# Kernel tuning notes

Measured on AMD Instinct MI355X. Metric: run time of the kernel, lower is better.

## Reference

```python
import jax, jax.numpy as jnp
import numpy as np

B, T, D = 128, 2048, 256


def setup_inputs() -> dict:
    key = jax.random.key(0)
    ks = jax.random.split(key, 6)
    s = 1.0 / np.sqrt(D)  # kaiming-uniform-ish scale for bias-free Linear
    return {
        "x": jax.random.normal(ks[0], (B, T, D), jnp.float32),
        "W_in": jax.random.normal(ks[1], (D, D), jnp.float32) * s,
        "W_select": jax.random.normal(ks[2], (D, D), jnp.float32) * s,
        "W_gate": jax.random.normal(ks[3], (D, D), jnp.float32) * s,
        "W_out": jax.random.normal(ks[4], (D, D), jnp.float32) * s,
        "W_delta": jax.random.normal(ks[5], (D, D), jnp.float32) * s,
        "log_a": jnp.zeros((D,), jnp.float32),  # module inits log_a = zeros
    }


def _diag_recurrence(decay, update):
    # state_t = decay_t * state_{t-1} + update_t, state_{-1} = 0 (zero-init fast path)
    # First-order linear recurrence as an associative scan:
    # (a1,b1) o (a2,b2) = (a1*a2, a2*b1 + b2)
    def combine(c1, c2):
        a1, b1 = c1
        a2, b2 = c2
        return a1 * a2, a2 * b1 + b2

    _, states = jax.lax.associative_scan(combine, (decay, update), axis=1)
    return states  # (B, T, D)


def reference(x, W_in, W_select, W_gate, W_out, W_delta, log_a):
    # selective diag-SSM (a_mode='diag'):
    #   delta  = softplus(delta_proj(x))                  timestep / selectivity
    #   decay  = exp(-delta * exp(log_a))                 in (0, 1]
    #   update = delta * sigmoid(select_proj(x)) * in_proj(x)
    #   states = scan(state = decay*state + update)
    #   y      = states * silu(gate_proj(x)); out = out_proj(y)
    delta = jax.nn.softplus(jnp.einsum("btd,ed->bte", x, W_delta))
    decay = jnp.exp(-delta * jnp.exp(log_a))
    u = jnp.einsum("btd,ed->bte", x, W_in)
    sel = jax.nn.sigmoid(jnp.einsum("btd,ed->bte", x, W_select))
    update = delta * sel * u
    states = _diag_recurrence(decay, update)
    gate = jax.nn.silu(jnp.einsum("btd,ed->bte", x, W_gate))
    return jnp.einsum("btd,ed->bte", states * gate, W_out)
```

## Files before the change

kernel.cpp:

```cpp
#include <hip/hip_runtime.h>
#include <hip/hip_bf16.h>
#include <hip/hip_fp16.h>
#include <math.h>


typedef __attribute__((ext_vector_type(8))) short s16x8;
typedef __attribute__((ext_vector_type(4))) float f32x4;

#define D_DIM 256
#define T_DIM 2048
#define B_DIM 128
#define NCHUNK2 32
#define CLEN 128

__device__ __forceinline__ unsigned short f2bf(float f) {
    union { float f; unsigned int u; } v; v.f = f;
    unsigned int r = v.u + 0x7fffu + ((v.u >> 16) & 1u);
    return (unsigned short)(r >> 16);
}
__device__ __forceinline__ float bf2f(unsigned short s) {
    union { unsigned int u; float f; } v; v.u = ((unsigned int)s) << 16;
    return v.f;
}
__device__ __forceinline__ void gload_lds16(const void* g, void* l) {
    __builtin_amdgcn_global_load_lds(
        (const __attribute__((address_space(1))) unsigned int*)g,
        (__attribute__((address_space(3))) unsigned int*)l, 16, 0, 0);
}

__global__ __launch_bounds__(256) void prep_kernel(
    const float* __restrict__ W_in, const float* __restrict__ W_select,
    const float* __restrict__ W_gate, const float* __restrict__ W_out,
    const float* __restrict__ W_delta, const float* __restrict__ log_a,
    unsigned short* __restrict__ Wb, float* __restrict__ ea)
{
    int i = blockIdx.x * 256 + threadIdx.x;
    if (i < 4 * 65536) {
        int row = i >> 8, k = i & 255;
        int n = row >> 2, w = row & 3;
        const float* src = (w == 0) ? W_delta : (w == 1) ? W_select
                         : (w == 2) ? W_in    : W_gate;
        Wb[i] = f2bf(src[n * 256 + k]);
    } else if (i < 5 * 65536) {
        Wb[i] = f2bf(W_out[i - 4 * 65536]);
    } else if (i < 5 * 65536 + 256) {
        int j = i - 5 * 65536;
        ea[j] = expf(log_a[j]);
    }
}

__global__ __launch_bounds__(256) void xcast_kernel(
    const float* __restrict__ x, unsigned short* __restrict__ xb)
{
    size_t i = ((size_t)blockIdx.x * 256 + threadIdx.x) * 8;
    float4 p0 = *(const float4*)(x + i);
    float4 p1 = *(const float4*)(x + i + 4);
    s16x8 a;
    a[0] = (short)f2bf(p0.x); a[1] = (short)f2bf(p0.y);
    a[2] = (short)f2bf(p0.z); a[3] = (short)f2bf(p0.w);
    a[4] = (short)f2bf(p1.x); a[5] = (short)f2bf(p1.y);
    a[6] = (short)f2bf(p1.z); a[7] = (short)f2bf(p1.w);
    *(s16x8*)(xb + i) = a;
}

__global__ __launch_bounds__(256, 3) void gemm_fused_kernel(
    const unsigned short* __restrict__ xb, const unsigned short* __restrict__ Wcat,
    const float* __restrict__ ea,
    __half2* __restrict__ du, unsigned short* __restrict__ gate,
    float* __restrict__ cA, float* __restrict__ cS)
{
    __shared__ char lds[32768];
    int bid = blockIdx.x;
    int wg  = (bid & 7) * 2048 + (bid >> 3);
    int mt  = wg >> 3;
    int nt  = wg & 7;
    int mbase = mt * 128;
    int nb = nt * 128;
    int tid = threadIdx.x, lane = tid & 63, wid = tid >> 6;
    int l16 = lane & 15, lk = lane >> 4;
    int wr = wid >> 1, wc = wid & 1;

    const unsigned short* xg  = xb   + (size_t)mbase * D_DIM;
    const unsigned short* wgp = Wcat + (size_t)nb * D_DIM;

    int se0 = tid, se1 = 256 + tid;
    int sr0 = se0 >> 2, sg0 = (se0 & 3) ^ ((sr0 >> 1) & 3);
    int sr1 = se1 >> 2, sg1 = (se1 & 3) ^ ((sr1 >> 1) & 3);

    float eav[4];
#pragma unroll
    for (int nf = 0; nf < 4; ++nf)
        eav[nf] = ea[nt * 32 + wc * 16 + nf * 4 + lk];
    asm volatile("s_waitcnt vmcnt(0)" ::: "memory");
    __builtin_amdgcn_sched_barrier(0);

#define STAGE(BUFB, KB)                                                     \
    {                                                                        \
        gload_lds16(xg  + (size_t)sr0 * D_DIM + (KB) + sg0 * 8,              \
                    lds + (BUFB) + se0 * 16);                                \
        gload_lds16(xg  + (size_t)sr1 * D_DIM + (KB) + sg1 * 8,              \
                    lds + (BUFB) + se1 * 16);                                \
        gload_lds16(wgp + (size_t)sr0 * D_DIM + (KB) + sg0 * 8,              \
                    lds + (BUFB) + 8192 + se0 * 16);                         \
        gload_lds16(wgp + (size_t)sr1 * D_DIM + (KB) + sg1 * 8,              \
                    lds + (BUFB) + 8192 + se1 * 16);                         \
    }

    f32x4 acc[4][4] = {};

#define COMPUTE(BUFB)                                                        \
    {                                                                        \
        s16x8 xf[4], wf[4];                                                  \
        _Pragma("unroll")                                                    \
        for (int mf = 0; mf < 4; ++mf) {                                     \
            int row = wr * 64 + mf * 16 + l16;                               \
            int g = lk ^ ((row >> 1) & 3);                                   \
            xf[mf] = *(const s16x8*)(lds + (BUFB) + row * 64 + g * 16);      \
        }                                                                    \
        _Pragma("unroll")                                                    \
        for (int nf = 0; nf < 4; ++nf) {                                     \
            int row = wc * 64 + nf * 16 + l16;                               \
            int g = lk ^ ((row >> 1) & 3);                                   \
            wf[nf] = *(const s16x8*)(lds + (BUFB) + 8192 + row * 64 + g * 16);\
        }                                                                    \
        _Pragma("unroll")                                                    \
        for (int nf = 0; nf < 4; ++nf)                                       \
            _Pragma("unroll")                                                \
            for (int mf = 0; mf < 4; ++mf)                                   \
                acc[mf][nf] = __builtin_amdgcn_mfma_f32_16x16x32_bf16(       \
                    wf[nf], xf[mf], acc[mf][nf], 0, 0, 0);                   \
    }

    STAGE(0, 0);
#pragma unroll 1
    for (int p = 0; p < 4; ++p) {
        STAGE(16384, (2 * p + 1) * 32);
        __builtin_amdgcn_sched_barrier(0);
        asm volatile("s_waitcnt vmcnt(4)" ::: "memory");
        __builtin_amdgcn_s_barrier();
        __builtin_amdgcn_sched_barrier(0);
        COMPUTE(0);
        __builtin_amdgcn_sched_barrier(0);
        asm volatile("s_waitcnt lgkmcnt(0)" ::: "memory");
        __builtin_amdgcn_s_barrier();
        __builtin_amdgcn_sched_barrier(0);
        if (p < 3) {
            STAGE(0, (2 * p + 2) * 32);
            __builtin_amdgcn_sched_barrier(0);
            asm volatile("s_waitcnt vmcnt(4)" ::: "memory");
        } else {
            __builtin_amdgcn_sched_barrier(0);
            asm volatile("s_waitcnt vmcnt(0)" ::: "memory");
        }
        __builtin_amdgcn_s_barrier();
        __builtin_amdgcn_sched_barrier(0);
        COMPUTE(16384);
        __builtin_amdgcn_sched_barrier(0);
        asm volatile("s_waitcnt lgkmcnt(0)" ::: "memory");
        __builtin_amdgcn_s_barrier();
        __builtin_amdgcn_sched_barrier(0);
    }
#undef STAGE
#undef COMPUTE

#pragma unroll
    for (int nf = 0; nf < 4; ++nf) {
        int n = nt * 32 + wc * 16 + nf * 4 + lk;
        float ean = eav[nf];
        float A[4], S[4];
#pragma unroll
        for (int mf = 0; mf < 4; ++mf) {
            int m = mbase + wr * 64 + mf * 16 + l16;
            float zd = acc[mf][nf][0];
            float zs = acc[mf][nf][1];
            float zi = acc[mf][nf][2];
            float zg = acc[mf][nf][3];
            float e = __expf(zd);
            float delta = (zd > 15.f) ? zd : __logf(1.f + e);
            float dec = __expf(-delta * ean);
            float sel = 1.f / (1.f + __expf(-zs));
            float upd = delta * sel * zi;
            float g   = zg / (1.f + __expf(-zg));
            du[(size_t)m * D_DIM + n] = __floats2half2_rn(dec, upd);
            gate[(size_t)m * D_DIM + n] = f2bf(g);
            A[mf] = dec;
            S[mf] = upd;
        }
#pragma unroll
        for (int d = 1; d < 16; d <<= 1) {
            bool upper = (l16 & d);
#pragma unroll
            for (int mf = 0; mf < 4; ++mf) {
                float Ap = __shfl_xor(A[mf], d, 64);
                float Sp = __shfl_xor(S[mf], d, 64);
                float Se = upper ? Sp : S[mf];
                float Al = upper ? A[mf] : Ap;
                float Sl = upper ? S[mf] : Sp;
                S[mf] = fmaf(Al, Se, Sl);
                A[mf] = A[mf] * Ap;
            }
        }
        float cAe = A[0], cSe = S[0];
#pragma unroll
        for (int mf = 1; mf < 4; ++mf) {
            cSe = fmaf(A[mf], cSe, S[mf]);
            cAe *= A[mf];
        }
        if (l16 == 0) {
            int hc = mt * 2 + wr;
            cA[hc * D_DIM + n] = cAe;
            cS[hc * D_DIM + n] = cSe;
        }
    }
}

__global__ __launch_bounds__(256) void scan2_kernel(
    const float* __restrict__ cA, const float* __restrict__ cS,
    float* __restrict__ carry)
{
    int b = blockIdx.x;
    int d = threadIdx.x;
    float s = 0.f;
    for (int c = 0; c < NCHUNK2; ++c) {
        int idx = (b * NCHUNK2 + c) * D_DIM + d;
        carry[idx] = s;
        s = fmaf(cA[idx], s, cS[idx]);
    }
}

__global__ __launch_bounds__(256) void scan_out_kernel(
    const __half2* __restrict__ du, const unsigned short* __restrict__ gate,
    const float* __restrict__ carry, const unsigned short* __restrict__ Wo,
    float* __restrict__ out)
{
    __shared__ unsigned short yls[128 * 256];
    int b = blockIdx.x >> 4;
    int c = blockIdx.x & 15;
    int tid = threadIdx.x;

    {
        int d = tid;
        size_t base = ((size_t)b * T_DIM + (size_t)c * CLEN) * D_DIM + d;
        float s = carry[(b * NCHUNK2 + c * 2) * D_DIM + d];
        int dlo = d & 7, dch = d >> 3;
#pragma unroll 4
        for (int t = 0; t < CLEN; ++t) {
            __half2 v = du[base + (size_t)t * D_DIM];
            float dc = __low2float(v);
            float up = __high2float(v);
            s = fmaf(dc, s, up);
            float g = bf2f(gate[base + (size_t)t * D_DIM]);
            int off = t * 256 + ((dch ^ (t & 7)) << 3) + dlo;
            yls[off] = f2bf(s * g);
        }
    }
    __syncthreads();

    int lane = tid & 63, wid = tid >> 6;
    int l16 = lane & 15;
    int lkc = lane >> 4;
    int m0 = (wid >> 1) * 64;
    size_t rbase = (size_t)b * T_DIM + (size_t)c * CLEN;
    int r0 = lkc * 4;

    for (int nblk = 0; nblk < 2; ++nblk) {
        int n0 = (wid & 1) * 64 + nblk * 128;
        f32x4 acc[4][4] = {};
        for (int ks = 0; ks < 8; ++ks) {
            int kb = ks * 32 + lkc * 8;
            s16x8 yf[4];
#pragma unroll
            for (int mf = 0; mf < 4; ++mf) {
                int row = m0 + mf * 16 + l16;
                int chunk = (ks * 4 + lkc) ^ (row & 7);
                yf[mf] = *(const s16x8*)&yls[row * 256 + chunk * 8];
            }
#pragma unroll
            for (int nf = 0; nf < 4; ++nf) {
                s16x8 wfr = *(const s16x8*)(Wo + (size_t)(n0 + nf * 16 + l16) * D_DIM + kb);
#pragma unroll
                for (int mf = 0; mf < 4; ++mf)
                    acc[mf][nf] = __builtin_amdgcn_mfma_f32_16x16x32_bf16(
                        wfr, yf[mf], acc[mf][nf], 0, 0, 0);
            }
        }
#pragma unroll
        for (int mf = 0; mf < 4; ++mf) {
            size_t rowg = rbase + m0 + mf * 16 + l16;
#pragma unroll
            for (int nf = 0; nf < 4; ++nf) {
                int n = n0 + nf * 16 + r0;
                *(f32x4*)(out + rowg * D_DIM + n) = acc[mf][nf];
            }
        }
    }
}

extern "C" void kernel_launch(void* const* d_in, const int* in_sizes, int n_in,
                              void* d_out, int out_size, void* d_ws, size_t ws_size,
                              hipStream_t stream)
{
    const float* x        = (const float*)d_in[0];
    const float* W_in     = (const float*)d_in[1];
    const float* W_select = (const float*)d_in[2];
    const float* W_gate   = (const float*)d_in[3];
    const float* W_out    = (const float*)d_in[4];
    const float* W_delta  = (const float*)d_in[5];
    const float* log_a    = (const float*)d_in[6];
    float* out = (float*)d_out;

    char* ws = (char*)d_ws;
    const size_t MB = 1ull << 20;
    unsigned short* Wb    = (unsigned short*)(ws);
    float*          ea    = (float*)(ws + 655360);
    unsigned short* xb    = (unsigned short*)(ws + 1 * MB);
    __half2*        du    = (__half2*)(ws + 129 * MB);
    unsigned short* gate  = (unsigned short*)(ws + 385 * MB);
    float*          cA    = (float*)(ws + 513 * MB);
    float*          cS    = (float*)(ws + 517 * MB);
    float*          carry = (float*)(ws + 521 * MB);

    prep_kernel<<<1281, 256, 0, stream>>>(W_in, W_select, W_gate, W_out,
                                          W_delta, log_a, Wb, ea);
    xcast_kernel<<<32768, 256, 0, stream>>>(x, xb);
    gemm_fused_kernel<<<16384, 256, 0, stream>>>(xb, Wb, ea, du, gate, cA, cS);
    scan2_kernel<<<B_DIM, 256, 0, stream>>>(cA, cS, carry);
    scan_out_kernel<<<B_DIM * NCHUNK2 / 2, 256, 0, stream>>>(du, gate, carry,
                                                             Wb + 4 * 65536, out);
}
```

Baseline: 674.6 us.

## Triple-buffer GEMM K-loop with precomputed LDS offsets and MFMA priority

Replaces the double-buffered K loop in the fused projection GEMM with a fully unrolled triple-buffered pipeline, keeping two global-to-LDS stages in flight while computing. Per-lane LDS fragment offsets are hoisted out of the compute macro, and wave priority is raised around the MFMA block. Global load latency should hide better, at the cost of 48KB of LDS per block, which may pressure occupancy.

```diff
diff --git a/kernel.cpp b/kernel.cpp
--- a/kernel.cpp
+++ b/kernel.cpp
@@ -69,7 +69,7 @@
     __half2* __restrict__ du, unsigned short* __restrict__ gate,
     float* __restrict__ cA, float* __restrict__ cS)
 {
-    __shared__ char lds[32768];
+    __shared__ char lds[49152];
     int bid = blockIdx.x;
     int wg  = (bid & 7) * 2048 + (bid >> 3);
     int mt  = wg >> 3;
@@ -87,6 +87,18 @@
     int sr0 = se0 >> 2, sg0 = (se0 & 3) ^ ((sr0 >> 1) & 3);
     int sr1 = se1 >> 2, sg1 = (se1 & 3) ^ ((sr1 >> 1) & 3);
 
+    int xoff[4], woff[4];
+#pragma unroll
+    for (int mf = 0; mf < 4; ++mf) {
+        int row = wr * 64 + mf * 16 + l16;
+        xoff[mf] = row * 64 + (lk ^ ((row >> 1) & 3)) * 16;
+    }
+#pragma unroll
+    for (int nf = 0; nf < 4; ++nf) {
+        int row = wc * 64 + nf * 16 + l16;
+        woff[nf] = 8192 + row * 64 + (lk ^ ((row >> 1) & 3)) * 16;
+    }
+
     float eav[4];
 #pragma unroll
     for (int nf = 0; nf < 4; ++nf)
@@ -94,7 +106,7 @@
     asm volatile("s_waitcnt vmcnt(0)" ::: "memory");
     __builtin_amdgcn_sched_barrier(0);
 
-#define STAGE(BUFB, KB)                                                     \
+#define STAGE(BUFB, KB)                                                      \
     {                                                                        \
         gload_lds16(xg  + (size_t)sr0 * D_DIM + (KB) + sg0 * 8,              \
                     lds + (BUFB) + se0 * 16);                                \
@@ -112,56 +124,47 @@
     {                                                                        \
         s16x8 xf[4], wf[4];                                                  \
         _Pragma("unroll")                                                    \
-        for (int mf = 0; mf < 4; ++mf) {                                     \
-            int row = wr * 64 + mf * 16 + l16;                               \
-            int g = lk ^ ((row >> 1) & 3);                                   \
-            xf[mf] = *(const s16x8*)(lds + (BUFB) + row * 64 + g * 16);      \
-        }                                                                    \
+        for (int mf = 0; mf < 4; ++mf)                                       \
+            xf[mf] = *(const s16x8*)(lds + (BUFB) + xoff[mf]);               \
         _Pragma("unroll")                                                    \
-        for (int nf = 0; nf < 4; ++nf) {                                     \
-            int row = wc * 64 + nf * 16 + l16;                               \
-            int g = lk ^ ((row >> 1) & 3);                                   \
-            wf[nf] = *(const s16x8*)(lds + (BUFB) + 8192 + row * 64 + g * 16);\
-        }                                                                    \
+        for (int nf = 0; nf < 4; ++nf)                                       \
+            wf[nf] = *(const s16x8*)(lds + (BUFB) + woff[nf]);               \
+        __builtin_amdgcn_s_setprio(1);                                       \
         _Pragma("unroll")                                                    \
         for (int nf = 0; nf < 4; ++nf)                                       \
             _Pragma("unroll")                                                \
             for (int mf = 0; mf < 4; ++mf)                                   \
                 acc[mf][nf] = __builtin_amdgcn_mfma_f32_16x16x32_bf16(       \
                     wf[nf], xf[mf], acc[mf][nf], 0, 0, 0);                   \
-    }
+        __builtin_amdgcn_s_setprio(0);                                       \
+    }
+
+#define SYNC_IN(VMSTR)                                                       \
+    __builtin_amdgcn_sched_barrier(0);                                       \
+    asm volatile("s_waitcnt vmcnt(" VMSTR ")" ::: "memory");                 \
+    __builtin_amdgcn_s_barrier();                                            \
+    __builtin_amdgcn_sched_barrier(0);
+
+#define SYNC_OUT                                                             \
+    __builtin_amdgcn_sched_barrier(0);                                       \
+    asm volatile("s_waitcnt lgkmcnt(0)" ::: "memory");                       \
+    __builtin_amdgcn_s_barrier();                                            \
+    __builtin_amdgcn_sched_barrier(0);
 
     STAGE(0, 0);
-#pragma unroll 1
-    for (int p = 0; p < 4; ++p) {
-        STAGE(16384, (2 * p + 1) * 32);
-        __builtin_amdgcn_sched_barrier(0);
-        asm volatile("s_waitcnt vmcnt(4)" ::: "memory");
-        __builtin_amdgcn_s_barrier();
-        __builtin_amdgcn_sched_barrier(0);
-        COMPUTE(0);
-        __builtin_amdgcn_sched_barrier(0);
-        asm volatile("s_waitcnt lgkmcnt(0)" ::: "memory");
-        __builtin_amdgcn_s_barrier();
-        __builtin_amdgcn_sched_barrier(0);
-        if (p < 3) {
-            STAGE(0, (2 * p + 2) * 32);
-            __builtin_amdgcn_sched_barrier(0);
-            asm volatile("s_waitcnt vmcnt(4)" ::: "memory");
-        } else {
-            __builtin_amdgcn_sched_barrier(0);
-            asm volatile("s_waitcnt vmcnt(0)" ::: "memory");
-        }
-        __builtin_amdgcn_s_barrier();
-        __builtin_amdgcn_sched_barrier(0);
-        COMPUTE(16384);
-        __builtin_amdgcn_sched_barrier(0);
-        asm volatile("s_waitcnt lgkmcnt(0)" ::: "memory");
-        __builtin_amdgcn_s_barrier();
-        __builtin_amdgcn_sched_barrier(0);
-    }
+    STAGE(16384, 32);
+    STAGE(32768, 64);   SYNC_IN("8")  COMPUTE(0)      SYNC_OUT
+    STAGE(0, 96);       SYNC_IN("8")  COMPUTE(16384)  SYNC_OUT
+    STAGE(16384, 128);  SYNC_IN("8")  COMPUTE(32768)  SYNC_OUT
+    STAGE(32768, 160);  SYNC_IN("8")  COMPUTE(0)      SYNC_OUT
+    STAGE(0, 192);      SYNC_IN("8")  COMPUTE(16384)  SYNC_OUT
+    STAGE(16384, 224);  SYNC_IN("8")  COMPUTE(32768)  SYNC_OUT
+                        SYNC_IN("4")  COMPUTE(0)      SYNC_OUT
+                        SYNC_IN("0")  COMPUTE(16384)  SYNC_OUT
 #undef STAGE
 #undef COMPUTE
+#undef SYNC_IN
+#undef SYNC_OUT
 
 #pragma unroll
     for (int nf = 0; nf < 4; ++nf) {
```

After: 671.8 us. No clear change (-0.4%).
